# Kernel optimization log

Hardware: AMD Instinct MI355X
Metric: run time of the kernel (lower is better)

The kernel has to match this reference:

```python
import jax, jax.numpy as jnp
import numpy as np

B, T, I = 256, 256, 32
H, O, F = 512, 32, 128


def setup_inputs() -> dict:
    key = jax.random.key(0)
    ks = jax.random.split(key, 7)
    s = 1.0 / np.sqrt(H)
    return {
        "x": jax.random.normal(ks[0], (B, T, I), dtype=jnp.float32),
        "W_ih": jax.random.uniform(ks[1], (4 * H, I), jnp.float32, -s, s),
        "W_hh": jax.random.uniform(ks[2], (4 * H, H), jnp.float32, -s, s),
        "b_ih": jax.random.uniform(ks[3], (4 * H,), jnp.float32, -s, s),
        "b_hh": jax.random.uniform(ks[4], (4 * H,), jnp.float32, -s, s),
        "W_fc": jax.random.uniform(ks[5], (O, H), jnp.float32, -s, s),
        "b_fc": jax.random.uniform(ks[6], (O,), jnp.float32, -s, s),
        "future_steps": F,
    }


def _lstm_cell(h, c, x_t, W_ih, W_hh, b):
    # PyTorch gate layout: [i, f, g, o] stacked along 4H
    gates = x_t @ W_ih.T + h @ W_hh.T + b  # [B, 4H]
    i, f, g, o = jnp.split(gates, 4, axis=-1)
    c_new = jax.nn.sigmoid(f) * c + jax.nn.sigmoid(i) * jnp.tanh(g)
    h_new = jax.nn.sigmoid(o) * jnp.tanh(c_new)
    return h_new, c_new


def reference(x, W_ih, W_hh, b_ih, b_hh, W_fc, b_fc, future_steps):
    b = b_ih + b_hh
    Bx = x.shape[0]
    h0 = jnp.zeros((Bx, H), x.dtype)
    c0 = jnp.zeros((Bx, H), x.dtype)

    # ---- encoder: run LSTM over the input sequence ----
    def enc_step(carry, x_t):
        h, c = carry
        h, c = _lstm_cell(h, c, x_t, W_ih, W_hh, b)
        return (h, c), None

    (h, c), _ = jax.lax.scan(enc_step, (h0, c0), jnp.swapaxes(x, 0, 1))

    pred = h @ W_fc.T + b_fc  # [B, O] prediction for next step

    def dec_step(carry, _):
        h, c, pred = carry
        out = pred  # appended BEFORE the lstm step, as in the torch loop
        h, c = _lstm_cell(h, c, pred, W_ih, W_hh, b)
        pred_next = h @ W_fc.T + b_fc
        return (h, c, pred_next), out

    _, preds = jax.lax.scan(dec_step, (h, c, pred), None, length=future_steps)
    return jnp.swapaxes(preds, 0, 1)  # [B, future_steps, O]
```

## Files before the change

kernel.cpp:

```cpp
#include <hip/hip_runtime.h>
#include <cmath>

#define TSEQ  256
#define ISZ   32
#define HSZ   512
#define OSZ   32
#define FUT   128

typedef float  f32x4 __attribute__((ext_vector_type(4)));
typedef short  s16x8 __attribute__((ext_vector_type(8)));
typedef unsigned int   uint32;
typedef unsigned int   u32x4 __attribute__((ext_vector_type(4)));
typedef unsigned short u16;

#define MFMA_BF16 __builtin_amdgcn_mfma_f32_16x16x32_bf16

__device__ __forceinline__ float sigm(float v) { return 1.0f / (1.0f + __expf(-v)); }

template<int OFF>
__device__ __forceinline__ u32x4 ldH_cc(const uint32* p) {
    u32x4 d;
    asm volatile("global_load_dwordx4 %0, %1, off offset:%2 sc0 sc1"
                 : "=v"(d) : "v"(p), "n"(OFF) : "memory");
    return d;
}
template<int OFF>
__device__ __forceinline__ f32x4 ldX(const float* p) {
    f32x4 d;
    asm volatile("global_load_dwordx4 %0, %1, off offset:%2"
                 : "=v"(d) : "v"(p), "n"(OFF) : "memory");
    return d;
}
__device__ __forceinline__ void st32_cc(uint32* p, uint32 v) {
    asm volatile("global_store_dword %0, %1, off sc0 sc1" :: "v"(p), "v"(v) : "memory");
}
__device__ __forceinline__ uint32 ld32_cc(const uint32* p) {
    uint32 d;
    asm volatile("global_load_dword %0, %1, off sc0 sc1" : "=v"(d) : "v"(p) : "memory");
    return d;
}
#define WAITV(N) do { asm volatile("s_waitcnt vmcnt(" #N ")" ::: "memory"); \
                      __builtin_amdgcn_sched_barrier(0); } while (0)

__device__ __forceinline__ void split8(const float* p, s16x8& hi, s16x8& lo) {
    float v[8];
    *(f32x4*)&v[0] = *(const f32x4*)p;
    *(f32x4*)&v[4] = *(const f32x4*)(p + 4);
    uint32* ph = (uint32*)&hi; uint32* pl = (uint32*)&lo;
    #pragma unroll
    for (int q = 0; q < 4; ++q) {
        uint32 u0 = __float_as_uint(v[2*q]),   h0 = u0 & 0xFFFF0000u;
        uint32 u1 = __float_as_uint(v[2*q+1]), h1 = u1 & 0xFFFF0000u;
        float r0 = v[2*q]   - __uint_as_float(h0);
        float r1 = v[2*q+1] - __uint_as_float(h1);
        ph[q] = (h0 >> 16) | h1;
        pl[q] = (__float_as_uint(r0) >> 16) | (__float_as_uint(r1) & 0xFFFF0000u);
    }
}

__global__ __launch_bounds__(512) void prep_weights(
    const float* __restrict__ Whh, const float* __restrict__ Wih,
    const float* __restrict__ Wfc, const float* __restrict__ bih,
    const float* __restrict__ bhh, const float* __restrict__ bfc,
    u16* WhpH, u16* WhpL, u16* WfcH, u16* WfcL,
    float* bsum, float* bsumP)
{
    const int r = (int)blockIdx.x;
    const int k = (int)threadIdx.x;
    float acc = Whh[(size_t)r * HSZ + k];
    #pragma unroll 8
    for (int i = 0; i < ISZ; ++i)
        acc += Wih[r * ISZ + i] * Wfc[i * HSZ + k];
    {
        uint32 u = __float_as_uint(acc), hu = u & 0xFFFF0000u;
        float rs = acc - __uint_as_float(hu);
        WhpH[(size_t)r * HSZ + k] = (u16)(u >> 16);
        WhpL[(size_t)r * HSZ + k] = (u16)(__float_as_uint(rs) >> 16);
    }
    if (r < OSZ) {
        float v = Wfc[r * HSZ + k];
        uint32 u = __float_as_uint(v), hu = u & 0xFFFF0000u;
        float rs = v - __uint_as_float(hu);
        WfcH[r * HSZ + k] = (u16)(u >> 16);
        WfcL[r * HSZ + k] = (u16)(__float_as_uint(rs) >> 16);
    }
    if (k == 0) {
        float b = bih[r] + bhh[r];
        float bp = b;
        #pragma unroll 8
        for (int i = 0; i < ISZ; ++i) bp += Wih[r * ISZ + i] * bfc[i];
        bsum[r] = b; bsumP[r] = bp;
    }
}

__global__ __launch_bounds__(512, 1) void lstm_mfma5(
    const float* __restrict__ x,
    const float* __restrict__ Whh32, const float* __restrict__ Wih32,
    const float* __restrict__ b_fc,
    float* __restrict__ out,
    const u16* __restrict__ WhpHg, const u16* __restrict__ WhpLg,
    const u16* __restrict__ WfcHg, const u16* __restrict__ WfcLg,
    const float* __restrict__ bsum, const float* __restrict__ bsumP,
    uint32* hG0, uint32* hG1, uint32* flg)
{
    __shared__ __align__(16) u16 bHi[2][16][256];
    __shared__ __align__(16) u16 bLo[2][16][256];
    __shared__ float gatebuf[128][17];

    const int tid  = (int)threadIdx.x;
    const int cg   = (int)blockIdx.x & 15;
    const int rg   = (int)blockIdx.x >> 4;
    const int w    = tid >> 6, lane = tid & 63;
    const int ks   = lane >> 4, lcol = lane & 15;
    const bool dopred = (rg == 0) && (w < 2);
    const int prow = w * 16 + lcol;

    const int grow = (w >> 1) * HSZ + rg * 32 + (w & 1) * 16 + lcol;

    s16x8 wH[16], wL[16];
    #pragma unroll
    for (int kt = 0; kt < 16; ++kt)
        split8(Whh32 + (size_t)grow * HSZ + kt * 32 + ks * 8, wH[kt], wL[kt]);
    s16x8 ihH, ihL;
    split8(Wih32 + (size_t)grow * ISZ + ks * 8, ihH, ihL);

    const int scol = tid >> 5, skb = tid & 31;
    const uint32* sb0 = hG0 + (size_t)(cg * 16 + scol) * HSZ + skb * 8;
    const uint32* sb1 = hG1 + (size_t)(cg * 16 + scol) * HSZ + skb * 8;
    const size_t hidx = (size_t)(cg * 16 + scol) * HSZ + rg * 32 + skb;
    uint32* hwA = hG1 + hidx;
    uint32* hwB = hG0 + hidx;

    const float biv = bsum [           rg * 32 + skb];
    const float bfv = bsum [    HSZ  + rg * 32 + skb];
    const float bgv = bsum [2 * HSZ  + rg * 32 + skb];
    const float bov = bsum [3 * HSZ  + rg * 32 + skb];
    const float biP = bsumP[           rg * 32 + skb];
    const float bfP = bsumP[    HSZ  + rg * 32 + skb];
    const float bgP = bsumP[2 * HSZ  + rg * 32 + skb];
    const float boP = bsumP[3 * HSZ  + rg * 32 + skb];
    float pbq[4] = {0.f, 0.f, 0.f, 0.f};
    if (w < 2) {
        #pragma unroll
        for (int q = 0; q < 4; ++q) pbq[q] = b_fc[w * 16 + ks * 4 + q];
    }

    const float* xbase = x + (size_t)(cg * 16 + lcol) * (TSEQ * ISZ) + ks * 8;
    float* outp = out + (size_t)(cg * 16 + lcol) * (FUT * OSZ);
    uint32* myflag = flg + ((cg * 16 + rg) << 4);

    float cst = 0.f;
    __syncthreads();

#define STAGE_WR(H)                                                            \
    { u32x4 v0 = sreg[(H) * 2], v1 = sreg[(H) * 2 + 1];                        \
      u32x4 hw_, lw_;                                                          \
      hw_[0] = (v0[0] >> 16) | (v0[1] & 0xFFFF0000u);                          \
      hw_[1] = (v0[2] >> 16) | (v0[3] & 0xFFFF0000u);                          \
      hw_[2] = (v1[0] >> 16) | (v1[1] & 0xFFFF0000u);                          \
      hw_[3] = (v1[2] >> 16) | (v1[3] & 0xFFFF0000u);                          \
      lw_[0] = (v0[0] & 0xFFFFu) | (v0[1] << 16);                              \
      lw_[1] = (v0[2] & 0xFFFFu) | (v0[3] << 16);                              \
      lw_[2] = (v1[0] & 0xFFFFu) | (v1[1] << 16);                              \
      lw_[3] = (v1[2] & 0xFFFFu) | (v1[3] << 16);                              \
      const int go = (skb ^ scol) << 3;                                        \
      *(u32x4*)&bHi[H][scol][go] = hw_;                                        \
      *(u32x4*)&bLo[H][scol][go] = lw_; }

#define CONS_KT(H, KTL)                                                        \
    { const int g = ((((KTL) * 4) + ks) ^ lcol) << 3;                          \
      s16x8 bh = *(const s16x8*)&bHi[H][lcol][g];                              \
      s16x8 bl = *(const s16x8*)&bLo[H][lcol][g];                              \
      gA = MFMA_BF16(wH[(H) * 8 + (KTL)], bh, gA, 0, 0, 0);                    \
      gB = MFMA_BF16(wH[(H) * 8 + (KTL)], bl, gB, 0, 0, 0);                    \
      gC = MFMA_BF16(wL[(H) * 8 + (KTL)], bh, gC, 0, 0, 0);                    \
      if (dec && dopred) {                                                     \
          s16x8 fh = *(const s16x8*)(WfcHg + (size_t)prow * HSZ                \
                                     + ((H) * 8 + (KTL)) * 32 + ks * 8);       \
          s16x8 fl = *(const s16x8*)(WfcLg + (size_t)prow * HSZ                \
                                     + ((H) * 8 + (KTL)) * 32 + ks * 8);       \
          pA = MFMA_BF16(fh, bh, pA, 0, 0, 0);                                 \
          pB = MFMA_BF16(fh, bl, pB, 0, 0, 0);                                 \
          pC = MFMA_BF16(fl, bh, pC, 0, 0, 0);                                 \
      } }
#define CONS_HALF(H) \
    CONS_KT(H,0) CONS_KT(H,1) CONS_KT(H,2) CONS_KT(H,3) \
    CONS_KT(H,4) CONS_KT(H,5) CONS_KT(H,6) CONS_KT(H,7)

    #pragma unroll 1
    for (int tt = 0; tt < TSEQ + FUT; ++tt) {
        const bool dec = (tt >= TSEQ);
        const uint32* sb = (tt & 1) ? sb1 : sb0;
        uint32* hwp = (tt & 1) ? hwB : hwA;

        if (tt == TSEQ) {
            #pragma unroll
            for (int kt = 0; kt < 16; ++kt) {
                wH[kt] = *(const s16x8*)(WhpHg + (size_t)grow * HSZ + kt * 32 + ks * 8);
                wL[kt] = *(const s16x8*)(WhpLg + (size_t)grow * HSZ + kt * 32 + ks * 8);
            }
        }

        f32x4 gA = {0,0,0,0}, gB = {0,0,0,0}, gC = {0,0,0,0};
        f32x4 pA = {0,0,0,0}, pB = {0,0,0,0}, pC = {0,0,0,0};
        f32x4 xv0 = {0,0,0,0}, xv1 = {0,0,0,0};
        u32x4 sreg[4];

        if (!dec) {
            const float* xp = xbase + (size_t)tt * ISZ;
            xv0 = ldX<0>(xp); xv1 = ldX<16>(xp);
        }
        sreg[0] = ldH_cc<0>(sb);    sreg[1] = ldH_cc<16>(sb);
        sreg[2] = ldH_cc<1024>(sb); sreg[3] = ldH_cc<1040>(sb);

        if (!dec) {
            WAITV(4);
            s16x8 xh, xl;
            float xv[8];
            *(f32x4*)&xv[0] = xv0; *(f32x4*)&xv[4] = xv1;
            split8(xv, xh, xl);
            gA = MFMA_BF16(ihH, xh, gA, 0, 0, 0);
            gB = MFMA_BF16(ihH, xl, gB, 0, 0, 0);
            gC = MFMA_BF16(ihL, xh, gC, 0, 0, 0);
        }

        WAITV(2);
        STAGE_WR(0);
        __syncthreads();
        CONS_HALF(0);
        WAITV(0);
        STAGE_WR(1);
        __syncthreads();
        CONS_HALF(1);

        if (dec && dopred) {
            f32x4 pr = pA + pB + pC;
            const int step = tt - TSEQ;
            #pragma unroll
            for (int q = 0; q < 4; ++q)
                outp[(size_t)step * OSZ + w * 16 + ks * 4 + q] = pr[q] + pbq[q];
        }

        f32x4 gt = gA + gB + gC;
        #pragma unroll
        for (int q = 0; q < 4; ++q)
            gatebuf[w * 16 + ks * 4 + q][lcol] = gt[q];
        __syncthreads();

        {
            float gi = gatebuf[      skb][scol] + (dec ? biP : biv);
            float gf = gatebuf[ 32 + skb][scol] + (dec ? bfP : bfv);
            float gg = gatebuf[ 64 + skb][scol] + (dec ? bgP : bgv);
            float go = gatebuf[ 96 + skb][scol] + (dec ? boP : bov);
            cst = sigm(gf) * cst + sigm(gi) * tanhf(gg);
            float hv = sigm(go) * tanhf(cst);
            uint32 u = __float_as_uint(hv), hu = u & 0xFFFF0000u;
            float rs = hv - __uint_as_float(hu);
            st32_cc(hwp, hu | (__float_as_uint(rs) >> 16));
        }

        WAITV(0);
        __syncthreads();
        const uint32 token = (uint32)tt + 1u;
        if (tid == 0) st32_cc(myflag, token);
        if (tid < 16) {
            const uint32* fp = flg + ((cg * 16 + tid) << 4);
            int guard = 0;
            for (;;) {
                uint32 v = ld32_cc(fp);
                WAITV(0);
                if (__all(v >= token) || guard > (1 << 13)) break;
                __builtin_amdgcn_s_sleep(1); ++guard;
            }
        }
        __syncthreads();
    }
#undef STAGE_WR
#undef CONS_KT
#undef CONS_HALF
}

extern "C" void kernel_launch(void* const* d_in, const int* in_sizes, int n_in,
                              void* d_out, int out_size, void* d_ws, size_t ws_size,
                              hipStream_t stream)
{
    (void)in_sizes; (void)n_in; (void)out_size; (void)ws_size;
    const float* x    = (const float*)d_in[0];
    const float* W_ih = (const float*)d_in[1];
    const float* W_hh = (const float*)d_in[2];
    const float* b_ih = (const float*)d_in[3];
    const float* b_hh = (const float*)d_in[4];
    const float* W_fc = (const float*)d_in[5];
    const float* b_fc = (const float*)d_in[6];
    float* out = (float*)d_out;

    char* ws = (char*)d_ws;
    uint32* flg  = (uint32*)(ws);
    uint32* hG0  = (uint32*)(ws + 16384);
    uint32* hG1  = (uint32*)(ws + 540672);
    u16* WhpH  = (u16*)(ws + 1064960);
    u16* WhpL  = (u16*)(ws + 3162112);
    u16* WfcH  = (u16*)(ws + 5259264);
    u16* WfcL  = (u16*)(ws + 5292032);
    float* bsum  = (float*)(ws + 5324800);
    float* bsumP = (float*)(ws + 5332992);

    hipMemsetAsync(ws, 0, 16384 + 524288, stream);

    prep_weights<<<2048, 512, 0, stream>>>(W_hh, W_ih, W_fc, b_ih, b_hh, b_fc,
                                           WhpH, WhpL, WfcH, WfcL, bsum, bsumP);

    lstm_mfma5<<<256, 512, 0, stream>>>(x, W_hh, W_ih, b_fc, out,
                                        WhpH, WhpL, WfcH, WfcL, bsum, bsumP,
                                        hG0, hG1, flg);
}
```

Measured before the change: 1.860 ms.

## Replace flag barrier with parity-tagged hidden state in a four-slot ring

Drops the separate per-block flag store and spin-wait. Each stored hidden value now carries a phase bit in its least-significant bit, and the state lives in a four-deep ring buffer. Consumers poll the hidden-state loads until every word shows the expected parity, which removes one global round trip and a block barrier per step. The cost is one mantissa bit of the bf16 low part, retry loops with extra block barriers whenever a poll fails, and both halves of the state now staged before the first MFMA, so load latency is no longer overlapped.

```diff
diff --git a/kernel.cpp b/kernel.cpp
--- a/kernel.cpp
+++ b/kernel.cpp
@@ -33,11 +33,6 @@
 }
 __device__ __forceinline__ void st32_cc(uint32* p, uint32 v) {
     asm volatile("global_store_dword %0, %1, off sc0 sc1" :: "v"(p), "v"(v) : "memory");
-}
-__device__ __forceinline__ uint32 ld32_cc(const uint32* p) {
-    uint32 d;
-    asm volatile("global_load_dword %0, %1, off sc0 sc1" : "=v"(d) : "v"(p) : "memory");
-    return d;
 }
 #define WAITV(N) do { asm volatile("s_waitcnt vmcnt(" #N ")" ::: "memory"); \
                       __builtin_amdgcn_sched_barrier(0); } while (0)
@@ -93,7 +88,7 @@
     }
 }
 
-__global__ __launch_bounds__(512, 1) void lstm_mfma5(
+__global__ __launch_bounds__(512, 1) void lstm_mfma6(
     const float* __restrict__ x,
     const float* __restrict__ Whh32, const float* __restrict__ Wih32,
     const float* __restrict__ b_fc,
@@ -101,11 +96,12 @@
     const u16* __restrict__ WhpHg, const u16* __restrict__ WhpLg,
     const u16* __restrict__ WfcHg, const u16* __restrict__ WfcLg,
     const float* __restrict__ bsum, const float* __restrict__ bsumP,
-    uint32* hG0, uint32* hG1, uint32* flg)
+    uint32* hBase)
 {
     __shared__ __align__(16) u16 bHi[2][16][256];
     __shared__ __align__(16) u16 bLo[2][16][256];
     __shared__ float gatebuf[128][17];
+    __shared__ int vfail;
 
     const int tid  = (int)threadIdx.x;
     const int cg   = (int)blockIdx.x & 15;
@@ -125,11 +121,8 @@
     split8(Wih32 + (size_t)grow * ISZ + ks * 8, ihH, ihL);
 
     const int scol = tid >> 5, skb = tid & 31;
-    const uint32* sb0 = hG0 + (size_t)(cg * 16 + scol) * HSZ + skb * 8;
-    const uint32* sb1 = hG1 + (size_t)(cg * 16 + scol) * HSZ + skb * 8;
-    const size_t hidx = (size_t)(cg * 16 + scol) * HSZ + rg * 32 + skb;
-    uint32* hwA = hG1 + hidx;
-    uint32* hwB = hG0 + hidx;
+    const size_t sboff = (size_t)(cg * 16 + scol) * HSZ + skb * 8;
+    const size_t hoff  = (size_t)(cg * 16 + scol) * HSZ + rg * 32 + skb;
 
     const float biv = bsum [           rg * 32 + skb];
     const float bfv = bsum [    HSZ  + rg * 32 + skb];
@@ -147,7 +140,6 @@
 
     const float* xbase = x + (size_t)(cg * 16 + lcol) * (TSEQ * ISZ) + ks * 8;
     float* outp = out + (size_t)(cg * 16 + lcol) * (FUT * OSZ);
-    uint32* myflag = flg + ((cg * 16 + rg) << 4);
 
     float cst = 0.f;
     __syncthreads();
@@ -190,8 +182,10 @@
     #pragma unroll 1
     for (int tt = 0; tt < TSEQ + FUT; ++tt) {
         const bool dec = (tt >= TSEQ);
-        const uint32* sb = (tt & 1) ? sb1 : sb0;
-        uint32* hwp = (tt & 1) ? hwB : hwA;
+        const uint32* sb = hBase + (size_t)((tt + 3) & 3) * 131072 + sboff;
+        uint32* hwp      = hBase + (size_t)(tt & 3)       * 131072 + hoff;
+        const uint32 wbit = (~((uint32)tt >> 2)) & 1u;
+        const uint32 exp  = (tt == 0) ? 0u : ((~(((uint32)tt - 1u) >> 2)) & 1u);
 
         if (tt == TSEQ) {
             #pragma unroll
@@ -210,11 +204,29 @@
             const float* xp = xbase + (size_t)tt * ISZ;
             xv0 = ldX<0>(xp); xv1 = ldX<16>(xp);
         }
-        sreg[0] = ldH_cc<0>(sb);    sreg[1] = ldH_cc<16>(sb);
-        sreg[2] = ldH_cc<1024>(sb); sreg[3] = ldH_cc<1040>(sb);
+
+        int guard = 0;
+        for (;;) {
+            sreg[0] = ldH_cc<0>(sb);    sreg[1] = ldH_cc<16>(sb);
+            sreg[2] = ldH_cc<1024>(sb); sreg[3] = ldH_cc<1040>(sb);
+            WAITV(0);
+            uint32 bad = 0;
+            #pragma unroll
+            for (int j = 0; j < 4; ++j) {
+                bad |= (sreg[j][0] ^ exp) | (sreg[j][1] ^ exp)
+                     | (sreg[j][2] ^ exp) | (sreg[j][3] ^ exp);
+            }
+            const bool ok = ((bad & 1u) == 0u);
+            if (tid == 0) vfail = 0;
+            __syncthreads();
+            if (!ok) vfail = 1;
+            __syncthreads();
+            if (vfail == 0) break;
+            if (++guard > 1024) break;
+            __builtin_amdgcn_s_sleep(1);
+        }
 
         if (!dec) {
-            WAITV(4);
             s16x8 xh, xl;
             float xv[8];
             *(f32x4*)&xv[0] = xv0; *(f32x4*)&xv[4] = xv1;
@@ -224,13 +236,10 @@
             gC = MFMA_BF16(ihL, xh, gC, 0, 0, 0);
         }
 
-        WAITV(2);
         STAGE_WR(0);
+        STAGE_WR(1);
         __syncthreads();
         CONS_HALF(0);
-        WAITV(0);
-        STAGE_WR(1);
-        __syncthreads();
         CONS_HALF(1);
 
         if (dec && dopred) {
@@ -256,22 +265,9 @@
             float hv = sigm(go) * tanhf(cst);
             uint32 u = __float_as_uint(hv), hu = u & 0xFFFF0000u;
             float rs = hv - __uint_as_float(hu);
-            st32_cc(hwp, hu | (__float_as_uint(rs) >> 16));
-        }
-
-        WAITV(0);
-        __syncthreads();
-        const uint32 token = (uint32)tt + 1u;
-        if (tid == 0) st32_cc(myflag, token);
-        if (tid < 16) {
-            const uint32* fp = flg + ((cg * 16 + tid) << 4);
-            int guard = 0;
-            for (;;) {
-                uint32 v = ld32_cc(fp);
-                WAITV(0);
-                if (__all(v >= token) || guard > (1 << 13)) break;
-                __builtin_amdgcn_s_sleep(1); ++guard;
-            }
+            uint32 pk = hu | (__float_as_uint(rs) >> 16);
+            pk = (pk & ~1u) | wbit;
+            st32_cc(hwp, pk);
         }
         __syncthreads();
     }
@@ -295,22 +291,20 @@
     float* out = (float*)d_out;
 
     char* ws = (char*)d_ws;
-    uint32* flg  = (uint32*)(ws);
-    uint32* hG0  = (uint32*)(ws + 16384);
-    uint32* hG1  = (uint32*)(ws + 540672);
-    u16* WhpH  = (u16*)(ws + 1064960);
-    u16* WhpL  = (u16*)(ws + 3162112);
-    u16* WfcH  = (u16*)(ws + 5259264);
-    u16* WfcL  = (u16*)(ws + 5292032);
-    float* bsum  = (float*)(ws + 5324800);
-    float* bsumP = (float*)(ws + 5332992);
-
-    hipMemsetAsync(ws, 0, 16384 + 524288, stream);
+    uint32* hBase = (uint32*)(ws);
+    u16* WhpH  = (u16*)(ws + (2048u  << 10));
+    u16* WhpL  = (u16*)(ws + (4096u  << 10));
+    u16* WfcH  = (u16*)(ws + (6144u  << 10));
+    u16* WfcL  = (u16*)(ws + (6176u  << 10));
+    float* bsum  = (float*)(ws + (6208u << 10));
+    float* bsumP = (float*)(ws + (6216u << 10));
+
+    hipMemsetAsync(ws + 3u * (512u << 10), 0, 512u << 10, stream);
 
     prep_weights<<<2048, 512, 0, stream>>>(W_hh, W_ih, W_fc, b_ih, b_hh, b_fc,
                                            WhpH, WhpL, WfcH, WfcL, bsum, bsumP);
 
-    lstm_mfma5<<<256, 512, 0, stream>>>(x, W_hh, W_ih, b_fc, out,
+    lstm_mfma6<<<256, 512, 0, stream>>>(x, W_hh, W_ih, b_fc, out,
                                         WhpH, WhpL, WfcH, WfcL, bsum, bsumP,
-                                        hG0, hG1, flg);
-}
+                                        hBase);
+}
```

Result: faster. 1.665 ms (-10.5%).

## Permute gate rows so each lane holds all four gates, dropping LDS transpose

Applied to the files above, without the earlier changes.

Reorders the W_hh/W_ih rows assigned to each MFMA output so that the four accumulator elements per lane are the i,f,g,o gates of one hidden unit. The cell update then reads gates straight from registers, which removes the shared-memory gatebuf round trip and one block-wide barrier per timestep. Hidden-state write addresses and bias indexing are remapped to match the new unit-per-lane layout. The global h stores are now scattered per lane instead of contiguous per row, which may cost some store efficiency.

```diff
diff --git a/kernel.cpp b/kernel.cpp
--- a/kernel.cpp
+++ b/kernel.cpp
@@ -93,7 +93,7 @@
     }
 }
 
-__global__ __launch_bounds__(512, 1) void lstm_mfma5(
+__global__ __launch_bounds__(512, 1) void lstm_mfma8(
     const float* __restrict__ x,
     const float* __restrict__ Whh32, const float* __restrict__ Wih32,
     const float* __restrict__ b_fc,
@@ -105,7 +105,6 @@
 {
     __shared__ __align__(16) u16 bHi[2][16][256];
     __shared__ __align__(16) u16 bLo[2][16][256];
-    __shared__ float gatebuf[128][17];
 
     const int tid  = (int)threadIdx.x;
     const int cg   = (int)blockIdx.x & 15;
@@ -115,7 +114,7 @@
     const bool dopred = (rg == 0) && (w < 2);
     const int prow = w * 16 + lcol;
 
-    const int grow = (w >> 1) * HSZ + rg * 32 + (w & 1) * 16 + lcol;
+    const int grow = (lcol & 3) * HSZ + rg * 32 + w * 4 + (lcol >> 2);
 
     s16x8 wH[16], wL[16];
     #pragma unroll
@@ -125,20 +124,23 @@
     split8(Wih32 + (size_t)grow * ISZ + ks * 8, ihH, ihL);
 
     const int scol = tid >> 5, skb = tid & 31;
-    const uint32* sb0 = hG0 + (size_t)(cg * 16 + scol) * HSZ + skb * 8;
-    const uint32* sb1 = hG1 + (size_t)(cg * 16 + scol) * HSZ + skb * 8;
-    const size_t hidx = (size_t)(cg * 16 + scol) * HSZ + rg * 32 + skb;
-    uint32* hwA = hG1 + hidx;
-    uint32* hwB = hG0 + hidx;
-
-    const float biv = bsum [           rg * 32 + skb];
-    const float bfv = bsum [    HSZ  + rg * 32 + skb];
-    const float bgv = bsum [2 * HSZ  + rg * 32 + skb];
-    const float bov = bsum [3 * HSZ  + rg * 32 + skb];
-    const float biP = bsumP[           rg * 32 + skb];
-    const float bfP = bsumP[    HSZ  + rg * 32 + skb];
-    const float bgP = bsumP[2 * HSZ  + rg * 32 + skb];
-    const float boP = bsumP[3 * HSZ  + rg * 32 + skb];
+    const size_t sboff = (size_t)(cg * 16 + scol) * HSZ + skb * 8;
+    const uint32* sb0 = hG0 + sboff;
+    const uint32* sb1 = hG1 + sboff;
+
+    const int unit = rg * 32 + w * 4 + ks;
+    const size_t hoff = (size_t)(cg * 16 + lcol) * HSZ + unit;
+    uint32* hwA = hG1 + hoff;
+    uint32* hwB = hG0 + hoff;
+
+    const float bi  = bsum [          unit];
+    const float bfv = bsum [    HSZ + unit];
+    const float bgv = bsum [2 * HSZ + unit];
+    const float bov = bsum [3 * HSZ + unit];
+    const float biP = bsumP[          unit];
+    const float bfP = bsumP[    HSZ + unit];
+    const float bgP = bsumP[2 * HSZ + unit];
+    const float boP = bsumP[3 * HSZ + unit];
     float pbq[4] = {0.f, 0.f, 0.f, 0.f};
     if (w < 2) {
         #pragma unroll
@@ -241,17 +243,12 @@
                 outp[(size_t)step * OSZ + w * 16 + ks * 4 + q] = pr[q] + pbq[q];
         }
 
-        f32x4 gt = gA + gB + gC;
-        #pragma unroll
-        for (int q = 0; q < 4; ++q)
-            gatebuf[w * 16 + ks * 4 + q][lcol] = gt[q];
-        __syncthreads();
-
         {
-            float gi = gatebuf[      skb][scol] + (dec ? biP : biv);
-            float gf = gatebuf[ 32 + skb][scol] + (dec ? bfP : bfv);
-            float gg = gatebuf[ 64 + skb][scol] + (dec ? bgP : bgv);
-            float go = gatebuf[ 96 + skb][scol] + (dec ? boP : bov);
+            f32x4 gt = gA + gB + gC;
+            float gi = gt[0] + (dec ? biP : bi);
+            float gf = gt[1] + (dec ? bfP : bfv);
+            float gg = gt[2] + (dec ? bgP : bgv);
+            float go = gt[3] + (dec ? boP : bov);
             cst = sigm(gf) * cst + sigm(gi) * tanhf(gg);
             float hv = sigm(go) * tanhf(cst);
             uint32 u = __float_as_uint(hv), hu = u & 0xFFFF0000u;
@@ -310,7 +307,7 @@
     prep_weights<<<2048, 512, 0, stream>>>(W_hh, W_ih, W_fc, b_ih, b_hh, b_fc,
                                            WhpH, WhpL, WfcH, WfcL, bsum, bsumP);
 
-    lstm_mfma5<<<256, 512, 0, stream>>>(x, W_hh, W_ih, b_fc, out,
+    lstm_mfma8<<<256, 512, 0, stream>>>(x, W_hh, W_ih, b_fc, out,
                                         WhpH, WhpL, WfcH, WfcL, bsum, bsumP,
                                         hG0, hG1, flg);
 }
```

Result: no change. 1.886 ms (+1.4%).
